# Kernel tuning notes

Hardware: AMD Instinct MI355X
Metric: run time of the kernel (lower is better)

The kernel has to match this reference:

```python
import jax, jax.numpy as jnp
import numpy as np

B, NCLASS, NSUPP = 4096, 1000, 64
NCHUNK = NSUPP * NSUPP  # 4096, x's feature dim


def setup_inputs() -> dict:
    key = jax.random.key(0)
    k1, k2, k3 = jax.random.split(key, 3)
    x = jax.random.normal(k1, (B, NCHUNK), dtype=jnp.float32)
    # torch .uniform_(-1, 1)
    wSupp = jax.random.uniform(k2, (NCLASS, NSUPP), dtype=jnp.float32, minval=-1.0, maxval=1.0)
    chunk_map = jax.random.randint(k3, (NCLASS, NSUPP), 0, NCHUNK, dtype=jnp.int32)
    return {"x": x, "wSupp": wSupp, "chunk_map": chunk_map}


def reference(x, wSupp, chunk_map):
    # sparse_support: for each class i, feat_i = sum_j x[:, chunk_map[i,j]] * wSupp[i,j]; out = exp(feat)
    gathered = x[:, chunk_map]                      # [B, nClass, nSupp] gather via index map
    feats = jnp.einsum('bcs,cs->bc', gathered, wSupp)  # weighted sum over support
    return jnp.exp(feats)                           # [B, nClass]
```

## Files before the change

### kernel.cpp

```cpp
#include <hip/hip_runtime.h>
#include <hip/hip_fp16.h>


constexpr int B_       = 4096;
constexpr int NCLASS_  = 1000;
constexpr int NSUPP_   = 64;
constexpr int NCHUNK_  = 4096;
constexpr int BT       = 16;
constexpr int BH       = BT / 2;
constexpr int THREADS_ = 1024;
constexpr int SG_      = NSUPP_ / 4;
constexpr size_t CMT_BYTES = (size_t)SG_ * NCLASS_ * 16;
constexpr size_t WS_NEEDED = 2 * CMT_BYTES;

__global__ __launch_bounds__(256)
void build_cw_kernel(const int*   __restrict__ cm,
                     const float* __restrict__ w,
                     int*         __restrict__ cmT,
                     float*       __restrict__ wT)
{
    const int t    = threadIdx.x;
    const int c    = blockIdx.x * 4 + (t >> 6);
    const int lane = t & 63;
    if (c >= NCLASS_) return;

    const int   idx = cm[c * NSUPP_ + lane];
    const float wv  = w [c * NSUPP_ + lane];
    const int   key = (idx - c) & 7;

    const unsigned long long below = ((unsigned long long)1 << lane) - 1ull;
    int j = 0;
    #pragma unroll
    for (int r = 0; r < 8; ++r) {
        const unsigned long long m = __ballot(key == r);
        if (key > r)  j += __popcll(m);
        if (key == r) j += __popcll(m & below);
    }

    const int dst = ((j >> 2) * NCLASS_ + c) * 4 + (j & 3);
    cmT[dst] = idx;
    wT [dst] = wv;
}

template <bool USET>
__device__ __forceinline__ void gather_half(
    const float4* __restrict__ t4,
    const float4* __restrict__ wT, const int4* __restrict__ cmT,
    const float* __restrict__ wSupp, const int* __restrict__ cmap,
    const int c, int4& ci, float4& wf, float acc[BH])
{
    for (int sg = 0; sg < SG_; ++sg) {
        float4 d0 = t4[ci.x], d1 = t4[ci.y], d2 = t4[ci.z], d3 = t4[ci.w];
        const float4 wv = wf;

        const int sgn = (sg + 1 < SG_) ? sg + 1 : SG_ - 1;
        if constexpr (USET) {
            ci = cmT[sgn * NCLASS_ + c];
            wf = wT [sgn * NCLASS_ + c];
        } else {
            ci = reinterpret_cast<const int4*>(cmap + c * NSUPP_)[sgn];
            wf = reinterpret_cast<const float4*>(wSupp + c * NSUPP_)[sgn];
        }

        const float4* dp[4]  = {&d0, &d1, &d2, &d3};
        const float   ws4[4] = {wv.x, wv.y, wv.z, wv.w};
        #pragma unroll
        for (int j = 0; j < 4; ++j) {
            const __half2* h = reinterpret_cast<const __half2*>(dp[j]);
            #pragma unroll
            for (int k = 0; k < 4; ++k) {
                const float2 f = __half22float2(h[k]);
                acc[2 * k]     = fmaf(f.x, ws4[j], acc[2 * k]);
                acc[2 * k + 1] = fmaf(f.y, ws4[j], acc[2 * k + 1]);
            }
        }
    }
}

template <bool USET>
__global__ __launch_bounds__(THREADS_, 4)
void supp_gather_kernel(const float* __restrict__ x,
                        const float* __restrict__ wSupp,
                        const int*   __restrict__ cmap,
                        const float4* __restrict__ wT,
                        const int4*   __restrict__ cmT,
                        float*       __restrict__ out)
{
    __shared__ __align__(16) __half2 tile[NCHUNK_ * 8];
    __half2* tlo = tile;
    __half2* thi = tile + NCHUNK_ * 4;

    const int t  = threadIdx.x;
    const int rb = blockIdx.x * BT;

    int4   ci;
    float4 wf;
    if (t < NCLASS_) {
        if constexpr (USET) { ci = cmT[t]; wf = wT[t]; }
        else {
            ci = reinterpret_cast<const int4*>(cmap + t * NSUPP_)[0];
            wf = reinterpret_cast<const float4*>(wSupp + t * NSUPP_)[0];
        }
    }

    #pragma unroll
    for (int p = 0; p < NCHUNK_ / THREADS_; ++p) {
        const int col = t + THREADS_ * p;
        float v[BH];
        #pragma unroll
        for (int bi = 0; bi < BH; ++bi)
            v[bi] = x[(size_t)(rb + bi) * NCHUNK_ + col];
        __half2 h[BH / 2];
        #pragma unroll
        for (int k = 0; k < BH / 2; ++k)
            h[k] = __floats2half2_rn(v[2 * k], v[2 * k + 1]);
        *reinterpret_cast<float4*>(&tlo[(size_t)col * 4]) =
            *reinterpret_cast<const float4*>(&h[0]);
    }
    __syncthreads();

    float hv[4 * BH];
    #pragma unroll
    for (int p = 0; p < NCHUNK_ / THREADS_; ++p) {
        const int col = t + THREADS_ * p;
        #pragma unroll
        for (int bi = 0; bi < BH; ++bi)
            hv[p * BH + bi] = x[(size_t)(rb + BH + bi) * NCHUNK_ + col];
    }
    __builtin_amdgcn_sched_barrier(0);

    float accl[BH];
    if (t < NCLASS_) {
        #pragma unroll
        for (int bi = 0; bi < BH; ++bi) accl[bi] = 0.f;
        gather_half<USET>(reinterpret_cast<const float4*>(tlo),
                          wT, cmT, wSupp, cmap, t, ci, wf, accl);
    }

    #pragma unroll
    for (int p = 0; p < NCHUNK_ / THREADS_; ++p) {
        const int col = t + THREADS_ * p;
        __half2 h[BH / 2];
        #pragma unroll
        for (int k = 0; k < BH / 2; ++k)
            h[k] = __floats2half2_rn(hv[p * BH + 2 * k], hv[p * BH + 2 * k + 1]);
        *reinterpret_cast<float4*>(&thi[(size_t)col * 4]) =
            *reinterpret_cast<const float4*>(&h[0]);
    }
    if (t < NCLASS_) {
        if constexpr (USET) { ci = cmT[t]; wf = wT[t]; }
        else {
            ci = reinterpret_cast<const int4*>(cmap + t * NSUPP_)[0];
            wf = reinterpret_cast<const float4*>(wSupp + t * NSUPP_)[0];
        }
    }
    __syncthreads();

    if (t < NCLASS_) {
        const int c = t;
        #pragma unroll
        for (int bi = 0; bi < BH; ++bi)
            out[(size_t)(rb + bi) * NCLASS_ + c] = __expf(accl[bi]);

        float acch[BH];
        #pragma unroll
        for (int bi = 0; bi < BH; ++bi) acch[bi] = 0.f;
        gather_half<USET>(reinterpret_cast<const float4*>(thi),
                          wT, cmT, wSupp, cmap, c, ci, wf, acch);

        #pragma unroll
        for (int bi = 0; bi < BH; ++bi)
            out[(size_t)(rb + BH + bi) * NCLASS_ + c] = __expf(acch[bi]);
    }
}

extern "C" void kernel_launch(void* const* d_in, const int* in_sizes, int n_in,
                              void* d_out, int out_size, void* d_ws, size_t ws_size,
                              hipStream_t stream) {
    const float* x  = (const float*)d_in[0];
    const float* w  = (const float*)d_in[1];
    const int*   cm = (const int*)d_in[2];
    float*       o  = (float*)d_out;

    int*   cmT = (int*)d_ws;
    float* wT  = (float*)((char*)d_ws + CMT_BYTES);

    const dim3 grid(B_ / BT);
    if (ws_size >= WS_NEEDED) {
        build_cw_kernel<<<dim3((NCLASS_ + 3) / 4), dim3(256), 0, stream>>>(
            cm, w, cmT, wT);
        supp_gather_kernel<true><<<grid, dim3(THREADS_), 0, stream>>>(
            x, w, cm, (const float4*)wT, (const int4*)cmT, o);
    } else {
        supp_gather_kernel<false><<<grid, dim3(THREADS_), 0, stream>>>(
            x, w, cm, (const float4*)wT, (const int4*)cmT, o);
    }
}
```

Baseline: 116.3 us.

## Preload support indices into registers and interleave gather with tile conversion

Result: slower. 132.9 us (+14.3%).

```diff
diff --git a/kernel.cpp b/kernel.cpp
--- a/kernel.cpp
+++ b/kernel.cpp
@@ -10,6 +10,7 @@
 constexpr int BH       = BT / 2;
 constexpr int THREADS_ = 1024;
 constexpr int SG_      = NSUPP_ / 4;
+constexpr int SGH_     = SG_ / 2;
 constexpr size_t CMT_BYTES = (size_t)SG_ * NCLASS_ * 16;
 constexpr size_t WS_NEEDED = 2 * CMT_BYTES;
 
@@ -42,40 +43,52 @@
     wT [dst] = wv;
 }
 
-template <bool USET>
-__device__ __forceinline__ void gather_half(
-    const float4* __restrict__ t4,
-    const float4* __restrict__ wT, const int4* __restrict__ cmT,
-    const float* __restrict__ wSupp, const int* __restrict__ cmap,
-    const int c, int4& ci, float4& wf, float acc[BH])
-{
-    for (int sg = 0; sg < SG_; ++sg) {
-        float4 d0 = t4[ci.x], d1 = t4[ci.y], d2 = t4[ci.z], d3 = t4[ci.w];
-        const float4 wv = wf;
-
-        const int sgn = (sg + 1 < SG_) ? sg + 1 : SG_ - 1;
-        if constexpr (USET) {
-            ci = cmT[sgn * NCLASS_ + c];
-            wf = wT [sgn * NCLASS_ + c];
-        } else {
-            ci = reinterpret_cast<const int4*>(cmap + c * NSUPP_)[sgn];
-            wf = reinterpret_cast<const float4*>(wSupp + c * NSUPP_)[sgn];
-        }
-
-        const float4* dp[4]  = {&d0, &d1, &d2, &d3};
-        const float   ws4[4] = {wv.x, wv.y, wv.z, wv.w};
-        #pragma unroll
-        for (int j = 0; j < 4; ++j) {
-            const __half2* h = reinterpret_cast<const __half2*>(dp[j]);
-            #pragma unroll
-            for (int k = 0; k < 4; ++k) {
-                const float2 f = __half22float2(h[k]);
-                acc[2 * k]     = fmaf(f.x, ws4[j], acc[2 * k]);
-                acc[2 * k + 1] = fmaf(f.y, ws4[j], acc[2 * k + 1]);
-            }
-        }
-    }
-}
+static __device__ __forceinline__ float2 hx2f(const float u) {
+    union U { float f; __half2 h; } uu;
+    uu.f = u;
+    return __half22float2(uu.h);
+}
+
+#define SUPP_FMA(dc, wc, A) {                          \
+    const float2 f_ = hx2f(dc);                        \
+    (A).x = fmaf(f_.x, (wc), (A).x);                   \
+    (A).y = fmaf(f_.y, (wc), (A).y); }
+
+#define GATHER_ONE(d, wc)                              \
+    SUPP_FMA((d).x, (wc), a0)                          \
+    SUPP_FMA((d).y, (wc), a1)                          \
+    SUPP_FMA((d).z, (wc), a2)                          \
+    SUPP_FMA((d).w, (wc), a3)
+
+#define GATHER_SG(t4, ci, wf) {                        \
+    const float4 d0_ = (t4)[(ci).x];                   \
+    const float4 d1_ = (t4)[(ci).y];                   \
+    const float4 d2_ = (t4)[(ci).z];                   \
+    const float4 d3_ = (t4)[(ci).w];                   \
+    GATHER_ONE(d0_, (wf).x)                            \
+    GATHER_ONE(d1_, (wf).y)                            \
+    GATHER_ONE(d2_, (wf).z)                            \
+    GATHER_ONE(d3_, (wf).w) }
+
+#define GATHER_Q0(t4)                                  \
+    GATHER_SG(t4, cw0, wv0) GATHER_SG(t4, cw1, wv1)    \
+    GATHER_SG(t4, cw2, wv2) GATHER_SG(t4, cw3, wv3)
+#define GATHER_Q1(t4)                                  \
+    GATHER_SG(t4, cw4, wv4) GATHER_SG(t4, cw5, wv5)    \
+    GATHER_SG(t4, cw6, wv6) GATHER_SG(t4, cw7, wv7)
+
+#define LOAD_CW_G(I, H)                                                      \
+    if constexpr (USET) {                                                    \
+        cw##I = cmT[((H) * SGH_ + I) * NCLASS_ + c];                         \
+        wv##I = wT [((H) * SGH_ + I) * NCLASS_ + c];                         \
+    } else {                                                                 \
+        cw##I = reinterpret_cast<const int4*>(cmap + c * NSUPP_)[(H) * SGH_ + I];   \
+        wv##I = reinterpret_cast<const float4*>(wSupp + c * NSUPP_)[(H) * SGH_ + I];\
+    }
+#define LOAD_CW_HALF(H)                                \
+    LOAD_CW_G(0, H) LOAD_CW_G(1, H) LOAD_CW_G(2, H)    \
+    LOAD_CW_G(3, H) LOAD_CW_G(4, H) LOAD_CW_G(5, H)    \
+    LOAD_CW_G(6, H) LOAD_CW_G(7, H)
 
 template <bool USET>
 __global__ __launch_bounds__(THREADS_, 4)
@@ -89,19 +102,16 @@
     __shared__ __align__(16) __half2 tile[NCHUNK_ * 8];
     __half2* tlo = tile;
     __half2* thi = tile + NCHUNK_ * 4;
+    const float4* tlo4 = reinterpret_cast<const float4*>(tlo);
+    const float4* thi4 = reinterpret_cast<const float4*>(thi);
 
     const int t  = threadIdx.x;
     const int rb = blockIdx.x * BT;
-
-    int4   ci;
-    float4 wf;
-    if (t < NCLASS_) {
-        if constexpr (USET) { ci = cmT[t]; wf = wT[t]; }
-        else {
-            ci = reinterpret_cast<const int4*>(cmap + t * NSUPP_)[0];
-            wf = reinterpret_cast<const float4*>(wSupp + t * NSUPP_)[0];
-        }
-    }
+    const int c  = t;
+
+    int4   cw0, cw1, cw2, cw3, cw4, cw5, cw6, cw7;
+    float4 wv0, wv1, wv2, wv3, wv4, wv5, wv6, wv7;
+    if (t < NCLASS_) { LOAD_CW_HALF(0) }
 
     #pragma unroll
     for (int p = 0; p < NCHUNK_ / THREADS_; ++p) {
@@ -110,18 +120,20 @@
         #pragma unroll
         for (int bi = 0; bi < BH; ++bi)
             v[bi] = x[(size_t)(rb + bi) * NCHUNK_ + col];
-        __half2 h[BH / 2];
+        __half2 h2v[BH / 2];
         #pragma unroll
         for (int k = 0; k < BH / 2; ++k)
-            h[k] = __floats2half2_rn(v[2 * k], v[2 * k + 1]);
+            h2v[k] = __floats2half2_rn(v[2 * k], v[2 * k + 1]);
         *reinterpret_cast<float4*>(&tlo[(size_t)col * 4]) =
-            *reinterpret_cast<const float4*>(&h[0]);
+            *reinterpret_cast<const float4*>(&h2v[0]);
     }
     __syncthreads();
 
-    float hv[4 * BH];
-    #pragma unroll
-    for (int p = 0; p < NCHUNK_ / THREADS_; ++p) {
+    float2 a0 = {0.f, 0.f}, a1 = {0.f, 0.f}, a2 = {0.f, 0.f}, a3 = {0.f, 0.f};
+    float hv[16];
+
+    #pragma unroll
+    for (int p = 0; p < 2; ++p) {
         const int col = t + THREADS_ * p;
         #pragma unroll
         for (int bi = 0; bi < BH; ++bi)
@@ -129,48 +141,71 @@
     }
     __builtin_amdgcn_sched_barrier(0);
 
-    float accl[BH];
+    if (t < NCLASS_) { GATHER_Q0(tlo4) }
+
+    #pragma unroll
+    for (int p = 0; p < 2; ++p) {
+        const int col = t + THREADS_ * p;
+        __half2 h2v[BH / 2];
+        #pragma unroll
+        for (int k = 0; k < BH / 2; ++k)
+            h2v[k] = __floats2half2_rn(hv[p * BH + 2 * k], hv[p * BH + 2 * k + 1]);
+        *reinterpret_cast<float4*>(&thi[(size_t)col * 4]) =
+            *reinterpret_cast<const float4*>(&h2v[0]);
+    }
+
+    #pragma unroll
+    for (int p = 0; p < 2; ++p) {
+        const int col = t + THREADS_ * (2 + p);
+        #pragma unroll
+        for (int bi = 0; bi < BH; ++bi)
+            hv[p * BH + bi] = x[(size_t)(rb + BH + bi) * NCHUNK_ + col];
+    }
+    __builtin_amdgcn_sched_barrier(0);
+
+    if (t < NCLASS_) { GATHER_Q1(tlo4) }
+
+    #pragma unroll
+    for (int p = 0; p < 2; ++p) {
+        const int col = t + THREADS_ * (2 + p);
+        __half2 h2v[BH / 2];
+        #pragma unroll
+        for (int k = 0; k < BH / 2; ++k)
+            h2v[k] = __floats2half2_rn(hv[p * BH + 2 * k], hv[p * BH + 2 * k + 1]);
+        *reinterpret_cast<float4*>(&thi[(size_t)col * 4]) =
+            *reinterpret_cast<const float4*>(&h2v[0]);
+    }
+
+    if (t < NCLASS_) { LOAD_CW_HALF(1) }
+    __syncthreads();
+
     if (t < NCLASS_) {
-        #pragma unroll
-        for (int bi = 0; bi < BH; ++bi) accl[bi] = 0.f;
-        gather_half<USET>(reinterpret_cast<const float4*>(tlo),
-                          wT, cmT, wSupp, cmap, t, ci, wf, accl);
-    }
-
-    #pragma unroll
-    for (int p = 0; p < NCHUNK_ / THREADS_; ++p) {
-        const int col = t + THREADS_ * p;
-        __half2 h[BH / 2];
-        #pragma unroll
-        for (int k = 0; k < BH / 2; ++k)
-            h[k] = __floats2half2_rn(hv[p * BH + 2 * k], hv[p * BH + 2 * k + 1]);
-        *reinterpret_cast<float4*>(&thi[(size_t)col * 4]) =
-            *reinterpret_cast<const float4*>(&h[0]);
-    }
-    if (t < NCLASS_) {
-        if constexpr (USET) { ci = cmT[t]; wf = wT[t]; }
-        else {
-            ci = reinterpret_cast<const int4*>(cmap + t * NSUPP_)[0];
-            wf = reinterpret_cast<const float4*>(wSupp + t * NSUPP_)[0];
-        }
-    }
-    __syncthreads();
-
-    if (t < NCLASS_) {
-        const int c = t;
-        #pragma unroll
-        for (int bi = 0; bi < BH; ++bi)
-            out[(size_t)(rb + bi) * NCLASS_ + c] = __expf(accl[bi]);
-
-        float acch[BH];
-        #pragma unroll
-        for (int bi = 0; bi < BH; ++bi) acch[bi] = 0.f;
-        gather_half<USET>(reinterpret_cast<const float4*>(thi),
-                          wT, cmT, wSupp, cmap, c, ci, wf, acch);
-
-        #pragma unroll
-        for (int bi = 0; bi < BH; ++bi)
-            out[(size_t)(rb + BH + bi) * NCLASS_ + c] = __expf(acch[bi]);
+        GATHER_Q0(tlo4)
+        GATHER_Q1(tlo4)
+        out[(size_t)(rb + 0) * NCLASS_ + c] = __expf(a0.x);
+        out[(size_t)(rb + 1) * NCLASS_ + c] = __expf(a0.y);
+        out[(size_t)(rb + 2) * NCLASS_ + c] = __expf(a1.x);
+        out[(size_t)(rb + 3) * NCLASS_ + c] = __expf(a1.y);
+        out[(size_t)(rb + 4) * NCLASS_ + c] = __expf(a2.x);
+        out[(size_t)(rb + 5) * NCLASS_ + c] = __expf(a2.y);
+        out[(size_t)(rb + 6) * NCLASS_ + c] = __expf(a3.x);
+        out[(size_t)(rb + 7) * NCLASS_ + c] = __expf(a3.y);
+
+        a0 = {0.f, 0.f}; a1 = {0.f, 0.f}; a2 = {0.f, 0.f}; a3 = {0.f, 0.f};
+        GATHER_Q0(thi4)
+        GATHER_Q1(thi4)
+
+        LOAD_CW_HALF(0)
+        GATHER_Q0(thi4)
+        GATHER_Q1(thi4)
+        out[(size_t)(rb +  8) * NCLASS_ + c] = __expf(a0.x);
+        out[(size_t)(rb +  9) * NCLASS_ + c] = __expf(a0.y);
+        out[(size_t)(rb + 10) * NCLASS_ + c] = __expf(a1.x);
+        out[(size_t)(rb + 11) * NCLASS_ + c] = __expf(a1.y);
+        out[(size_t)(rb + 12) * NCLASS_ + c] = __expf(a2.x);
+        out[(size_t)(rb + 13) * NCLASS_ + c] = __expf(a2.y);
+        out[(size_t)(rb + 14) * NCLASS_ + c] = __expf(a3.x);
+        out[(size_t)(rb + 15) * NCLASS_ + c] = __expf(a3.y);
     }
 }
 
```
